# Kernel optimization log

Hardware: AMD Instinct MI355X
Metric: run time of the kernel (lower is better)

## Reference

```python
import jax, jax.numpy as jnp
import numpy as np

B, L, V, D, N, K = 8, 512, 50257, 1024, 1024, 256


def setup_inputs() -> dict:
    key = jax.random.key(0)
    ks = jax.random.split(key, 8)
    s = 0.02
    return {
        "input_ids": jax.random.randint(ks[0], (B, L), 0, V, dtype=jnp.int32),
        "emb_inp": jax.random.normal(ks[1], (V, D), jnp.float32) * s,
        "W_ih": jax.random.normal(ks[2], (3 * D, D), jnp.float32) * s,   # rows ordered [r|z|n] like torch GRU
        "W_hh": jax.random.normal(ks[3], (3 * D, D), jnp.float32) * s,
        "b_ih": jnp.zeros((3 * D,), jnp.float32),
        "b_hh": jnp.zeros((3 * D,), jnp.float32),
        "W_A": jax.random.normal(ks[4], (N * K, D), jnp.float32) * s,    # ctx_to_A weight
        "b_A": jnp.zeros((N * K,), jnp.float32),
        "emb_geom": jax.random.normal(ks[5], (V, N), jnp.float32) * s,
    }


def reference(input_ids, emb_inp, W_ih, W_hh, b_ih, b_hh, W_A, b_A, emb_geom):
    # token embedding: (B, L, D)
    x = emb_inp[input_ids]
    # precompute input-side GRU gates once: (B, L, 3D)
    gi = jnp.einsum('bld,gd->blg', x, W_ih) + b_ih

    def step(h, gi_t):
        gh = h @ W_hh.T + b_hh                       # (B, 3D)
        ir, iz, i_n = jnp.split(gi_t, 3, axis=-1)
        hr, hz, h_n = jnp.split(gh, 3, axis=-1)
        r = jax.nn.sigmoid(ir + hr)
        z = jax.nn.sigmoid(iz + hz)
        n = jnp.tanh(i_n + r * h_n)
        h_new = (1.0 - z) * n + z * h                # torch GRU update
        return h_new, None

    h0 = jnp.zeros((x.shape[0], D), x.dtype)
    ctx_vec, _ = jax.lax.scan(step, h0, jnp.swapaxes(gi, 0, 1))  # final hidden (B, D)

    # context -> subspace basis U: (B, n, k)
    U = (ctx_vec @ W_A.T + b_A).reshape(-1, N, K)

    # scores[b,v] = e_v^T (U U^T) e_v == ||U^T e_v||^2  (rank-k rewrite, same math)
    Ue = jnp.einsum('vn,bnk->bvk', emb_geom, U)      # (B, V, K)
    logits = jnp.sum(Ue * Ue, axis=-1)               # (B, V)
    return logits
```

## Files before the change

### kernel.cpp

```cpp
#include <hip/hip_runtime.h>

#define D 1024
#define G3 3072
#define NV 50257
#define NU 1024
#define KU 256
#define TOKROWS 4096
#define SCL 256.0f
#define ISCL2 (1.0f / 65536.0f)
#define ISCL4 (1.0f / 4294967296.0f)

typedef __attribute__((ext_vector_type(8))) _Float16 half8;
typedef __attribute__((ext_vector_type(4))) _Float16 half4;
typedef __attribute__((ext_vector_type(4))) float f32x4;
typedef __attribute__((ext_vector_type(4))) unsigned u32x4;

#define GLDS16(gp, lp) __builtin_amdgcn_global_load_lds( \
    (const __attribute__((address_space(1))) void*)(const void*)(gp), \
    (__attribute__((address_space(3))) void*)(void*)(lp), 16, 0, 0)

static __device__ __forceinline__ float sigmoidf_(float x) {
  return 1.0f / (1.0f + __expf(-x));
}
static __device__ __forceinline__ float tanhf_(float x) {
  float e = __expf(2.0f * x);
  return 1.0f - 2.0f / (e + 1.0f);
}

__global__ __launch_bounds__(256) void k_prep(
    const int* __restrict__ ids, const float* __restrict__ emb,
    const float* __restrict__ Wih,
    _Float16* __restrict__ xh, _Float16* __restrict__ xl,
    _Float16* __restrict__ wh, _Float16* __restrict__ wl)
{
  int t = threadIdx.x;
  int wg = blockIdx.x;
  const float* src;
  _Float16 *dh, *dl;
  if (wg < TOKROWS) {
    src = emb + (size_t)ids[wg] * D;
    dh = xh + (size_t)wg * D; dl = xl + (size_t)wg * D;
  } else {
    int r = wg - TOKROWS;
    src = Wih + (size_t)r * D;
    dh = wh + (size_t)r * D; dl = wl + (size_t)r * D;
  }
  f32x4 v = ((const f32x4*)src)[t];
  half4 h, l;
#pragma unroll
  for (int j = 0; j < 4; ++j) {
    float vs = v[j] * SCL;
    _Float16 hi = (_Float16)vs;
    h[j] = hi;
    l[j] = (_Float16)(vs - (float)hi);
  }
  *(half4*)(dh + t * 4) = h;
  *(half4*)(dl + t * 4) = l;
}

__global__ __launch_bounds__(256) void k_gi(
    const _Float16* __restrict__ Ah, const _Float16* __restrict__ Al,
    const _Float16* __restrict__ Bh, const _Float16* __restrict__ Bl,
    const float* __restrict__ bih, float* __restrict__ gi)
{
  __shared__ _Float16 Ash[128 * 32];
  __shared__ _Float16 Asl[128 * 32];
  __shared__ _Float16 Bsh[128 * 32];
  __shared__ _Float16 Bsl[128 * 32];
  int tid = threadIdx.x;
  int bm = blockIdx.x, bn = blockIdx.y;
  int lane = tid & 63, w = tid >> 6;
  int nl = lane & 15, q = lane >> 4;
  int wr = w >> 1, wc = w & 1;
  f32x4 zero = {0.f, 0.f, 0.f, 0.f};
  f32x4 acc[4][4];
#pragma unroll
  for (int i = 0; i < 4; i++)
#pragma unroll
    for (int j = 0; j < 4; j++) acc[i][j] = zero;
  int r0 = tid >> 2;
  int c0 = (tid & 3) * 8;
  int wb = w * 512;
  for (int kc = 0; kc < 32; ++kc) {
    __syncthreads();
    size_t go = ((size_t)(bm * 128 + r0)) * D + kc * 32 + c0;
    size_t go2 = ((size_t)(bn * 128 + r0)) * D + kc * 32 + c0;
    GLDS16(Ah + go, Ash + wb);
    GLDS16(Ah + go + 64 * D, Ash + wb + 2048);
    GLDS16(Al + go, Asl + wb);
    GLDS16(Al + go + 64 * D, Asl + wb + 2048);
    GLDS16(Bh + go2, Bsh + wb);
    GLDS16(Bh + go2 + 64 * D, Bsh + wb + 2048);
    GLDS16(Bl + go2, Bsl + wb);
    GLDS16(Bl + go2 + 64 * D, Bsl + wb + 2048);
    __syncthreads();
    half8 afh[4], afl[4], bfh[4], bfl[4];
#pragma unroll
    for (int mt = 0; mt < 4; ++mt) {
      int o = (wr * 64 + mt * 16 + nl) * 32 + q * 8;
      afh[mt] = *(const half8*)(Ash + o);
      afl[mt] = *(const half8*)(Asl + o);
    }
#pragma unroll
    for (int nt = 0; nt < 4; ++nt) {
      int o = (wc * 64 + nt * 16 + nl) * 32 + q * 8;
      bfh[nt] = *(const half8*)(Bsh + o);
      bfl[nt] = *(const half8*)(Bsl + o);
    }
#pragma unroll
    for (int mt = 0; mt < 4; ++mt)
#pragma unroll
      for (int nt = 0; nt < 4; ++nt) {
        acc[mt][nt] = __builtin_amdgcn_mfma_f32_16x16x32_f16(afh[mt], bfh[nt], acc[mt][nt], 0, 0, 0);
        acc[mt][nt] = __builtin_amdgcn_mfma_f32_16x16x32_f16(afh[mt], bfl[nt], acc[mt][nt], 0, 0, 0);
        acc[mt][nt] = __builtin_amdgcn_mfma_f32_16x16x32_f16(afl[mt], bfh[nt], acc[mt][nt], 0, 0, 0);
      }
  }
#pragma unroll
  for (int mt = 0; mt < 4; ++mt)
#pragma unroll
    for (int nt = 0; nt < 4; ++nt) {
      int col = bn * 128 + wc * 64 + nt * 16 + nl;
      float bv = bih[col];
#pragma unroll
      for (int i = 0; i < 4; i++) {
        int row = bm * 128 + wr * 64 + mt * 16 + q * 4 + i;
        gi[(size_t)row * G3 + col] = acc[mt][nt][i] * ISCL2 + bv;
      }
    }
}

__global__ void k_init(unsigned* __restrict__ rec32)
{
  int t = threadIdx.x;
  for (int i = t; i < 32768; i += 256) rec32[i] = 0u;
}

__global__ __launch_bounds__(384) void k_gru(
    const float* __restrict__ Whh, const float* __restrict__ gi,
    const float* __restrict__ bhh, unsigned* __restrict__ hrec,
    float* __restrict__ ctx)
{
  int tid = threadIdx.x;
  int wid = blockIdx.x;
  int w = tid >> 6;
  int g = w >> 1;
  int kh = w & 1;
  int lane = tid & 63, nl = lane & 15, q = lane >> 4;
  __shared__ _Float16 hs[16 * 1024];
  __shared__ float gp[6][3][8][17];

  half8 bwh[16], bwl[16];
  {
    const float* wrow = Whh + ((size_t)(g * 1024 + wid * 16 + nl)) * D + kh * 512;
#pragma unroll
    for (int kt = 0; kt < 16; ++kt) {
      const f32x4* p = (const f32x4*)(wrow + kt * 32 + q * 8);
      f32x4 v0 = p[0], v1 = p[1];
      half8 h, l;
#pragma unroll
      for (int j = 0; j < 4; ++j) {
        float s0 = v0[j] * SCL;
        _Float16 h0 = (_Float16)s0;
        h[j] = h0; l[j] = (_Float16)(s0 - (float)h0);
        float s1 = v1[j] * SCL;
        _Float16 h1 = (_Float16)s1;
        h[j + 4] = h1; l[j + 4] = (_Float16)(s1 - (float)h1);
      }
      bwh[kt] = h; bwl[kt] = l;
    }
  }

  int m = tid >> 3, np = (tid & 7) * 2;
  int d0 = wid * 16 + np;
  float hr0 = 0.f, hr1 = 0.f;
  float bh[6] = {0, 0, 0, 0, 0, 0};
  if (tid < 64) {
#pragma unroll
    for (int gg = 0; gg < 3; ++gg) {
      bh[gg * 2] = bhh[gg * 1024 + d0];
      bh[gg * 2 + 1] = bhh[gg * 1024 + d0 + 1];
    }
  }
  f32x4 zero = {0, 0, 0, 0};

  for (int step = 0; step < 512; ++step) {
    float gi6[6] = {0, 0, 0, 0, 0, 0};
    if (tid < 64) {
      const float* gpt = gi + ((size_t)(m * 512 + step)) * G3 + d0;
#pragma unroll
      for (int gg = 0; gg < 3; ++gg) {
        gi6[gg * 2] = gpt[gg * 1024];
        gi6[gg * 2 + 1] = gpt[gg * 1024 + 1];
      }
    }

    {
      unsigned want = (unsigned)step;
      const u32x4* rb = (const u32x4*)hrec + (size_t)(step & 1) * 4096;
      u32x4 rv[11];
      unsigned need = 0;
#pragma unroll
      for (int k = 0; k < 11; ++k) {
        int r = tid + k * 384;
        if (r < 4096) need |= (1u << k);
      }
      while (need) {
        unsigned mm = need;
#pragma unroll
        for (int k = 0; k < 11; ++k)
          if (mm & (1u << k)) {
            int r = tid + k * 384;
            asm volatile("global_load_dwordx4 %0, %1, off sc0 sc1"
                         : "=v"(rv[k]) : "v"(rb + r));
          }
        asm volatile("s_waitcnt vmcnt(0)" ::: "memory");
#pragma unroll
        for (int k = 0; k < 11; ++k)
          if ((mm & (1u << k)) && rv[k][2] == want) need &= ~(1u << k);
      }
      __builtin_amdgcn_sched_barrier(0);
#pragma unroll
      for (int k = 0; k < 11; ++k) {
        int r = tid + k * 384;
        if (r < 4096) {
          int w2 = r >> 6, l2 = r & 63;
          int m2 = l2 >> 3;
          int d = (w2 << 4) + ((l2 & 7) << 1);
          int chunk = d >> 3, wi = d & 7;
          int sw = chunk ^ (m2 & 7);
          *(unsigned*)&hs[((m2 * 128 + sw) << 3) + wi] = rv[k][0];
          *(unsigned*)&hs[(((m2 + 8) * 128 + sw) << 3) + wi] = rv[k][1];
        }
      }
    }
    __syncthreads();

    half8 av[16];
#pragma unroll
    for (int kt = 0; kt < 16; ++kt) {
      int chunk = kh * 64 + kt * 4 + q;
      av[kt] = *(const half8*)&hs[(size_t)(nl * 128 + (chunk ^ (nl & 7))) * 8];
    }
    f32x4 ac1 = zero, ac2 = zero;
#pragma unroll
    for (int kt = 0; kt < 16; ++kt) {
      ac1 = __builtin_amdgcn_mfma_f32_16x16x32_f16(av[kt], bwh[kt], ac1, 0, 0, 0);
      ac2 = __builtin_amdgcn_mfma_f32_16x16x32_f16(av[kt], bwl[kt], ac2, 0, 0, 0);
    }
    if (q < 2) {
#pragma unroll
      for (int i = 0; i < 4; i++) {
        gp[w][0][q * 4 + i][nl] = ac1[i];
        gp[w][2][q * 4 + i][nl] = ac2[i];
      }
    } else {
#pragma unroll
      for (int i = 0; i < 4; i++) gp[w][1][(q - 2) * 4 + i][nl] = ac1[i];
    }
    __syncthreads();
    if (tid < 64) {
      float gh[6];
#pragma unroll
      for (int g2 = 0; g2 < 3; ++g2) {
        float s0 = 0.f, s1 = 0.f;
#pragma unroll
        for (int k2 = 0; k2 < 2; ++k2) {
          int wv = g2 * 2 + k2;
#pragma unroll
          for (int s = 0; s < 3; ++s) {
            s0 += gp[wv][s][m][np];
            s1 += gp[wv][s][m][np + 1];
          }
        }
        gh[g2 * 2] = s0 * ISCL2;
        gh[g2 * 2 + 1] = s1 * ISCL2;
      }
      float r0_ = sigmoidf_(gi6[0] + gh[0] + bh[0]);
      float r1_ = sigmoidf_(gi6[1] + gh[1] + bh[1]);
      float z0_ = sigmoidf_(gi6[2] + gh[2] + bh[2]);
      float z1_ = sigmoidf_(gi6[3] + gh[3] + bh[3]);
      float n0_ = tanhf_(gi6[4] + r0_ * (gh[4] + bh[4]));
      float n1_ = tanhf_(gi6[5] + r1_ * (gh[5] + bh[5]));
      float h0_ = (1.f - z0_) * n0_ + z0_ * hr0;
      float h1_ = (1.f - z1_) * n1_ + z1_ * hr1;
      hr0 = h0_; hr1 = h1_;
      float s0 = h0_ * SCL, s1 = h1_ * SCL;
      _Float16 h0h = (_Float16)s0, h1h = (_Float16)s1;
      _Float16 h0l = (_Float16)(s0 - (float)h0h), h1l = (_Float16)(s1 - (float)h1h);
      u32x4 rec;
      rec[0] = (unsigned)__builtin_bit_cast(unsigned short, h0h) |
               ((unsigned)__builtin_bit_cast(unsigned short, h1h) << 16);
      rec[1] = (unsigned)__builtin_bit_cast(unsigned short, h0l) |
               ((unsigned)__builtin_bit_cast(unsigned short, h1l) << 16);
      rec[2] = (unsigned)(step + 1);
      rec[3] = 0u;
      u32x4* dst = (u32x4*)hrec + ((size_t)((step + 1) & 1) * 4096 + wid * 64 + tid);
      asm volatile("global_store_dwordx4 %0, %1, off sc0 sc1"
                   :: "v"(dst), "v"(rec) : "memory");
      if (step == 511) {
        ctx[m * D + d0] = h0_;
        ctx[m * D + d0 + 1] = h1_;
      }
    }
  }
}

__global__ __launch_bounds__(256) void k_u(
    const float* __restrict__ WA, const float* __restrict__ bA,
    const float* __restrict__ ctx, _Float16* __restrict__ Uth,
    _Float16* __restrict__ Utl)
{
  __shared__ float As[128 * 32];
  __shared__ float cx[8][1032];
  int tid = threadIdx.x;
  int RB = blockIdx.x;
#pragma unroll
  for (int jj = 0; jj < 8; ++jj) {
    int e = tid * 32 + jj * 4;
    *(f32x4*)&cx[e >> 10][e & 1023] = *(const f32x4*)(ctx + e);
  }
  float acc[4] = {0.f, 0.f, 0.f, 0.f};
  int b = tid & 7, rq = tid >> 3;
  float* AsW = As + (tid >> 6) * 256;
  int sr = tid >> 3;
  int sc = (tid & 7) * 4;
  __syncthreads();
  for (int kc = 0; kc < 32; ++kc) {
    __syncthreads();
    const float* gsrc = WA + ((size_t)(RB * 128 + sr)) * D + kc * 32 + sc;
    GLDS16(gsrc, AsW);
    GLDS16(gsrc + 32 * D, AsW + 1024);
    GLDS16(gsrc + 64 * D, AsW + 2048);
    GLDS16(gsrc + 96 * D, AsW + 3072);
    __syncthreads();
    f32x4 cxr[8];
#pragma unroll
    for (int kk = 0; kk < 8; ++kk) cxr[kk] = *(const f32x4*)&cx[b][kc * 32 + kk * 4];
#pragma unroll
    for (int r = 0; r < 4; ++r) {
      const float* ap = As + (rq * 4 + r) * 32;
      float s = 0.f;
#pragma unroll
      for (int kk = 0; kk < 8; ++kk) {
        f32x4 a = *(const f32x4*)(ap + kk * 4);
        f32x4 c = cxr[kk];
        s += a[0] * c[0] + a[1] * c[1] + a[2] * c[2] + a[3] * c[3];
      }
      acc[r] += s;
    }
  }
#pragma unroll
  for (int r = 0; r < 4; ++r) {
    int R = RB * 128 + rq * 4 + r;
    float v = (acc[r] + bA[R]) * SCL;
    int n_u = R >> 8, k_u = R & 255;
    _Float16 hi = (_Float16)v;
    size_t o = ((size_t)(b * 256 + k_u)) * NU + n_u;
    Uth[o] = hi;
    Utl[o] = (_Float16)(v - (float)hi);
  }
}

__global__ __launch_bounds__(512, 1) void k_logits(
    const float* __restrict__ eg, const _Float16* __restrict__ Uth,
    const _Float16* __restrict__ Utl, float* __restrict__ out)
{
  __shared__ _Float16 Ash[128 * 40];
  __shared__ _Float16 Asl[128 * 40];
  __shared__ float lacc[8][128];
  int tid = threadIdx.x;
  int v0 = blockIdx.x * 128;
  int lane = tid & 63, w = tid >> 6, nl = lane & 15, q = lane >> 4;
  int bh = w & 1, wk = w >> 1;
  for (int i = tid; i < 1024; i += 512) ((float*)lacc)[i] = 0.f;
  int sr = tid >> 2;
  int sc = (tid & 3) * 8;
  int vr = v0 + sr;
  if (vr >= NV) vr = NV - 1;
  const float* asrc = eg + (size_t)vr * NU;
  f32x4 zero = {0, 0, 0, 0};
  __syncthreads();
  for (int kg = 0; kg < 4; ++kg) {
    f32x4 acc[4][8];
#pragma unroll
    for (int b = 0; b < 4; ++b)
#pragma unroll
      for (int mt = 0; mt < 8; ++mt) acc[b][mt] = zero;
    for (int nc = 0; nc < 32; ++nc) {
      __syncthreads();
      {
        const f32x4* p = (const f32x4*)(asrc + nc * 32 + sc);
        f32x4 u0 = p[0];
        f32x4 u1 = p[1];
        half8 h, l;
#pragma unroll
        for (int j = 0; j < 4; ++j) {
          float s0 = u0[j] * SCL;
          _Float16 h0 = (_Float16)s0;
          h[j] = h0; l[j] = (_Float16)(s0 - (float)h0);
          float s1 = u1[j] * SCL;
          _Float16 h1 = (_Float16)s1;
          h[j + 4] = h1; l[j + 4] = (_Float16)(s1 - (float)h1);
        }
        *(half8*)(Ash + sr * 40 + sc) = h;
        *(half8*)(Asl + sr * 40 + sc) = l;
      }
      __syncthreads();
      half8 afh[8], afl[8];
#pragma unroll
      for (int mt = 0; mt < 8; ++mt) {
        afh[mt] = *(const half8*)(Ash + (mt * 16 + nl) * 40 + q * 8);
        afl[mt] = *(const half8*)(Asl + (mt * 16 + nl) * 40 + q * 8);
      }
#pragma unroll
      for (int b = 0; b < 4; ++b) {
        int bb = bh * 4 + b;
        size_t o = ((size_t)(bb * 256 + kg * 64 + wk * 16 + nl)) * NU + nc * 32 + q * 8;
        half8 bfh = *(const half8*)(Uth + o);
        half8 bfl = *(const half8*)(Utl + o);
#pragma unroll
        for (int mt = 0; mt < 8; ++mt) {
          acc[b][mt] = __builtin_amdgcn_mfma_f32_16x16x32_f16(afh[mt], bfh, acc[b][mt], 0, 0, 0);
          acc[b][mt] = __builtin_amdgcn_mfma_f32_16x16x32_f16(afh[mt], bfl, acc[b][mt], 0, 0, 0);
          acc[b][mt] = __builtin_amdgcn_mfma_f32_16x16x32_f16(afl[mt], bfh, acc[b][mt], 0, 0, 0);
        }
      }
    }
#pragma unroll
    for (int b = 0; b < 4; ++b) {
      int bb = bh * 4 + b;
#pragma unroll
      for (int mt = 0; mt < 8; ++mt) {
#pragma unroll
        for (int i = 0; i < 4; ++i) {
          float s = acc[b][mt][i] * acc[b][mt][i];
          s += __shfl_xor(s, 1);
          s += __shfl_xor(s, 2);
          s += __shfl_xor(s, 4);
          s += __shfl_xor(s, 8);
          if (nl == 0) atomicAdd(&lacc[bb][mt * 16 + q * 4 + i], s);
        }
      }
    }
  }
  __syncthreads();
  if (tid < 128) {
    int v = v0 + tid;
    if (v < NV) {
#pragma unroll
      for (int b = 0; b < 8; ++b) out[(size_t)b * NV + v] = lacc[b][tid] * ISCL4;
    }
  }
}

extern "C" void kernel_launch(void* const* d_in, const int* in_sizes, int n_in,
                              void* d_out, int out_size, void* d_ws, size_t ws_size,
                              hipStream_t stream)
{
  (void)in_sizes; (void)n_in; (void)out_size; (void)ws_size;
  const int* ids = (const int*)d_in[0];
  const float* emb = (const float*)d_in[1];
  const float* Wih = (const float*)d_in[2];
  const float* Whh = (const float*)d_in[3];
  const float* bih = (const float*)d_in[4];
  const float* bhh = (const float*)d_in[5];
  const float* WA = (const float*)d_in[6];
  const float* bA = (const float*)d_in[7];
  const float* eg = (const float*)d_in[8];
  float* out = (float*)d_out;

  char* ws = (char*)d_ws;
  size_t off = 0;
  auto take = [&](size_t bytes) -> char* {
    char* p = ws + off;
    off += (bytes + 255) & ~(size_t)255;
    return p;
  };
  float* gi32 = (float*)take((size_t)4096 * 3072 * 4);
  char* xregion = take((size_t)4096 * 1024 * 2 * 2);
  _Float16* xh = (_Float16*)xregion;
  _Float16* xl = xh + (size_t)4096 * 1024;
  _Float16* wh = (_Float16*)take((size_t)3072 * 1024 * 2);
  _Float16* wl = (_Float16*)take((size_t)3072 * 1024 * 2);
  unsigned* hrec = (unsigned*)take((size_t)2 * 4096 * 16);
  float* ctx = (float*)take((size_t)8 * 1024 * 4);
  _Float16* Uth = (_Float16*)xregion;
  _Float16* Utl = Uth + (size_t)8 * 256 * 1024;

  k_prep<<<dim3(7168), dim3(256), 0, stream>>>(ids, emb, Wih, xh, xl, wh, wl);
  k_gi<<<dim3(32, 24), dim3(256), 0, stream>>>(xh, xl, wh, wl, bih, gi32);
  k_init<<<dim3(1), dim3(256), 0, stream>>>(hrec);
  k_gru<<<dim3(64), dim3(384), 0, stream>>>(Whh, gi32, bhh, hrec, ctx);
  k_u<<<dim3(2048), dim3(256), 0, stream>>>(WA, bA, ctx, Uth, Utl);
  k_logits<<<dim3(393), dim3(512), 0, stream>>>(eg, Uth, Utl, out);
}
```

Measured before the change: 3.059 ms.

## Widen gi GEMM K-tile with XOR-swizzled LDS and prefetch logits A-tile

Result: no change. 3.037 ms (-0.7%).

```diff
diff --git a/kernel.cpp b/kernel.cpp
--- a/kernel.cpp
+++ b/kernel.cpp
@@ -63,10 +63,10 @@
     const _Float16* __restrict__ Bh, const _Float16* __restrict__ Bl,
     const float* __restrict__ bih, float* __restrict__ gi)
 {
-  __shared__ _Float16 Ash[128 * 32];
-  __shared__ _Float16 Asl[128 * 32];
-  __shared__ _Float16 Bsh[128 * 32];
-  __shared__ _Float16 Bsl[128 * 32];
+  __shared__ _Float16 Ash[128 * 64];
+  __shared__ _Float16 Asl[128 * 64];
+  __shared__ _Float16 Bsh[128 * 64];
+  __shared__ _Float16 Bsl[128 * 64];
   int tid = threadIdx.x;
   int bm = blockIdx.x, bn = blockIdx.y;
   int lane = tid & 63, w = tid >> 6;
@@ -78,43 +78,52 @@
   for (int i = 0; i < 4; i++)
 #pragma unroll
     for (int j = 0; j < 4; j++) acc[i][j] = zero;
-  int r0 = tid >> 2;
-  int c0 = (tid & 3) * 8;
-  int wb = w * 512;
-  for (int kc = 0; kc < 32; ++kc) {
+  int srow_in = tid >> 3;
+  int cg = ((tid & 7) ^ (srow_in & 7)) * 8;
+  for (int kc = 0; kc < 16; ++kc) {
     __syncthreads();
-    size_t go = ((size_t)(bm * 128 + r0)) * D + kc * 32 + c0;
-    size_t go2 = ((size_t)(bn * 128 + r0)) * D + kc * 32 + c0;
-    GLDS16(Ah + go, Ash + wb);
-    GLDS16(Ah + go + 64 * D, Ash + wb + 2048);
-    GLDS16(Al + go, Asl + wb);
-    GLDS16(Al + go + 64 * D, Asl + wb + 2048);
-    GLDS16(Bh + go2, Bsh + wb);
-    GLDS16(Bh + go2 + 64 * D, Bsh + wb + 2048);
-    GLDS16(Bl + go2, Bsl + wb);
-    GLDS16(Bl + go2 + 64 * D, Bsl + wb + 2048);
+#pragma unroll
+    for (int s = 0; s < 4; ++s) {
+      size_t go = ((size_t)(bm * 128 + s * 32 + srow_in)) * D + kc * 64 + cg;
+      size_t go2 = ((size_t)(bn * 128 + s * 32 + srow_in)) * D + kc * 64 + cg;
+      int lb = s * 2048 + w * 512;
+      GLDS16(Ah + go, Ash + lb);
+      GLDS16(Al + go, Asl + lb);
+      GLDS16(Bh + go2, Bsh + lb);
+      GLDS16(Bl + go2, Bsl + lb);
+    }
     __syncthreads();
-    half8 afh[4], afl[4], bfh[4], bfl[4];
+    half8 afh[4][2], afl[4][2], bfh[4][2], bfl[4][2];
 #pragma unroll
     for (int mt = 0; mt < 4; ++mt) {
-      int o = (wr * 64 + mt * 16 + nl) * 32 + q * 8;
-      afh[mt] = *(const half8*)(Ash + o);
-      afl[mt] = *(const half8*)(Asl + o);
+      int R = wr * 64 + mt * 16 + nl;
+#pragma unroll
+      for (int kt = 0; kt < 2; ++kt) {
+        int o = R * 64 + ((kt * 4 + q) ^ (R & 7)) * 8;
+        afh[mt][kt] = *(const half8*)(Ash + o);
+        afl[mt][kt] = *(const half8*)(Asl + o);
+      }
     }
 #pragma unroll
     for (int nt = 0; nt < 4; ++nt) {
-      int o = (wc * 64 + nt * 16 + nl) * 32 + q * 8;
-      bfh[nt] = *(const half8*)(Bsh + o);
-      bfl[nt] = *(const half8*)(Bsl + o);
+      int R = wc * 64 + nt * 16 + nl;
+#pragma unroll
+      for (int kt = 0; kt < 2; ++kt) {
+        int o = R * 64 + ((kt * 4 + q) ^ (R & 7)) * 8;
+        bfh[nt][kt] = *(const half8*)(Bsh + o);
+        bfl[nt][kt] = *(const half8*)(Bsl + o);
+      }
     }
 #pragma unroll
     for (int mt = 0; mt < 4; ++mt)
 #pragma unroll
-      for (int nt = 0; nt < 4; ++nt) {
-        acc[mt][nt] = __builtin_amdgcn_mfma_f32_16x16x32_f16(afh[mt], bfh[nt], acc[mt][nt], 0, 0, 0);
-        acc[mt][nt] = __builtin_amdgcn_mfma_f32_16x16x32_f16(afh[mt], bfl[nt], acc[mt][nt], 0, 0, 0);
-        acc[mt][nt] = __builtin_amdgcn_mfma_f32_16x16x32_f16(afl[mt], bfh[nt], acc[mt][nt], 0, 0, 0);
-      }
+      for (int nt = 0; nt < 4; ++nt)
+#pragma unroll
+        for (int kt = 0; kt < 2; ++kt) {
+          acc[mt][nt] = __builtin_amdgcn_mfma_f32_16x16x32_f16(afh[mt][kt], bfh[nt][kt], acc[mt][nt], 0, 0, 0);
+          acc[mt][nt] = __builtin_amdgcn_mfma_f32_16x16x32_f16(afh[mt][kt], bfl[nt][kt], acc[mt][nt], 0, 0, 0);
+          acc[mt][nt] = __builtin_amdgcn_mfma_f32_16x16x32_f16(afl[mt][kt], bfh[nt][kt], acc[mt][nt], 0, 0, 0);
+        }
   }
 #pragma unroll
   for (int mt = 0; mt < 4; ++mt)
@@ -380,6 +389,8 @@
   if (vr >= NV) vr = NV - 1;
   const float* asrc = eg + (size_t)vr * NU;
   f32x4 zero = {0, 0, 0, 0};
+  f32x4 u0 = *(const f32x4*)(asrc + sc);
+  f32x4 u1 = *(const f32x4*)(asrc + sc + 4);
   __syncthreads();
   for (int kg = 0; kg < 4; ++kg) {
     f32x4 acc[4][8];
@@ -390,9 +401,6 @@
     for (int nc = 0; nc < 32; ++nc) {
       __syncthreads();
       {
-        const f32x4* p = (const f32x4*)(asrc + nc * 32 + sc);
-        f32x4 u0 = p[0];
-        f32x4 u1 = p[1];
         half8 h, l;
 #pragma unroll
         for (int j = 0; j < 4; ++j) {
@@ -406,6 +414,12 @@
         *(half8*)(Ash + sr * 40 + sc) = h;
         *(half8*)(Asl + sr * 40 + sc) = l;
       }
+      {
+        int nnc = (nc + 1) & 31;
+        const f32x4* np_ = (const f32x4*)(asrc + nnc * 32 + sc);
+        u0 = np_[0];
+        u1 = np_[1];
+      }
       __syncthreads();
       half8 afh[8], afl[8];
 #pragma unroll
@@ -413,6 +427,7 @@
         afh[mt] = *(const half8*)(Ash + (mt * 16 + nl) * 40 + q * 8);
         afl[mt] = *(const half8*)(Asl + (mt * 16 + nl) * 40 + q * 8);
       }
+      __builtin_amdgcn_s_setprio(1);
 #pragma unroll
       for (int b = 0; b < 4; ++b) {
         int bb = bh * 4 + b;
@@ -426,6 +441,7 @@
           acc[b][mt] = __builtin_amdgcn_mfma_f32_16x16x32_f16(afl[mt], bfh, acc[b][mt], 0, 0, 0);
         }
       }
+      __builtin_amdgcn_s_setprio(0);
     }
 #pragma unroll
     for (int b = 0; b < 4; ++b) {
```
